# Kernel optimization log

Measured on AMD Instinct MI355X. Metric: run time of the kernel, lower is better.

## Reference

```python
import jax, jax.numpy as jnp
import numpy as np

B, N, DIM = 8, 4096, 1024
H, DH = 16, 64          # heads, dim_head -> inner_dim = 1024
P = 256                 # proj_size (Linformer low-rank seq projection)
SCALE = DH ** -0.5


def setup_inputs() -> dict:
    key = jax.random.key(0)
    ks = jax.random.split(key, 6)
    return {
        "x": jax.random.normal(ks[0], (B, N, DIM), dtype=jnp.float32),
        "Wqkv": jax.random.normal(ks[1], (3 * H * DH, DIM), dtype=jnp.float32) * 0.02,
        "We": jax.random.normal(ks[2], (P, N), dtype=jnp.float32) * 0.02,
        "be": jax.random.normal(ks[3], (P,), dtype=jnp.float32) * 0.02,
        "Wo": jax.random.normal(ks[4], (DIM, H * DH), dtype=jnp.float32) * 0.02,
        "bo": jax.random.normal(ks[5], (DIM,), dtype=jnp.float32) * 0.02,
    }


def reference(x, Wqkv, We, be, Wo, bo):
    b, n, _ = x.shape
    # fused QKV projection (no bias), split, reshape to (b, h, n, d)
    qkv = jnp.einsum('bnc,ec->bne', x, Wqkv)                      # [b, n, 3*h*d]
    q, k, v = jnp.split(qkv, 3, axis=-1)
    tohead = lambda t: t.reshape(b, n, H, DH).transpose(0, 2, 1, 3)
    q, k, v = tohead(q), tohead(k), tohead(v)
    # shared E=F sequence projection: Linear over seq axis n -> p, bias along p
    kp = jnp.einsum('bhnd,pn->bhpd', k, We) + be[None, None, :, None]
    vp = jnp.einsum('bhnd,pn->bhpd', v, We) + be[None, None, :, None]
    dots = jnp.einsum('bhid,bhjd->bhij', q, kp) * SCALE           # [b, h, n, p]
    attn = jax.nn.softmax(dots, axis=-1)
    out = jnp.einsum('bhij,bhjd->bhid', attn, vp)                 # [b, h, n, d]
    out = out.transpose(0, 2, 1, 3).reshape(b, n, H * DH)
    return jnp.einsum('bne,oe->bno', out, Wo) + bo                # [b, n, dim]
```

## Files before the change

kernel.cpp:

```cpp
#include <hip/hip_runtime.h>
#include <hip/hip_bf16.h>


typedef unsigned short bf16u;
typedef __attribute__((ext_vector_type(8))) short short8;
typedef __attribute__((ext_vector_type(4))) float f32x4;

__device__ __forceinline__ unsigned short f2bf(float f) {
    unsigned u = __float_as_uint(f);
    u += 0x7FFF + ((u >> 16) & 1);
    return (unsigned short)(u >> 16);
}

__device__ __forceinline__ f32x4 mfma16(short8 a, short8 b, f32x4 c) {
    return __builtin_amdgcn_mfma_f32_16x16x32_bf16(a, b, c, 0, 0, 0);
}

__global__ void cvt_kernel(const float* __restrict__ in, bf16u* __restrict__ out, int n4) {
    int i = blockIdx.x * blockDim.x + threadIdx.x;
    int stride = gridDim.x * blockDim.x;
    for (int j = i; j < n4; j += stride) {
        float4 v = ((const float4*)in)[j];
        union { bf16u s[4]; uint2 u; } o;
        o.s[0] = f2bf(v.x); o.s[1] = f2bf(v.y); o.s[2] = f2bf(v.z); o.s[3] = f2bf(v.w);
        ((uint2*)out)[j] = o.u;
    }
}

__global__ __launch_bounds__(256) void cvt_transpose_x(const float* __restrict__ x,
                                                       bf16u* __restrict__ Xbf,
                                                       bf16u* __restrict__ XT) {
    __shared__ bf16u T[64][72];
    const int b = blockIdx.z;
    const int n0 = blockIdx.y * 64, c0 = blockIdx.x * 64;
    const int t = threadIdx.x;
    const int cx = t & 15, ry = t >> 4;
#pragma unroll
    for (int p = 0; p < 4; p++) {
        const int nn = p * 16 + ry;
        const size_t g = ((size_t)b * 4096 + n0 + nn) * 1024 + c0 + cx * 4;
        float4 v = *(const float4*)&x[g];
        union { bf16u s[4]; uint2 u; } o;
        o.s[0] = f2bf(v.x); o.s[1] = f2bf(v.y); o.s[2] = f2bf(v.z); o.s[3] = f2bf(v.w);
        *(uint2*)&Xbf[g] = o.u;
#pragma unroll
        for (int j = 0; j < 4; j++) T[cx * 4 + j][nn] = o.s[j];
    }
    __syncthreads();
    const int cc = t >> 2, ch = t & 3;
#pragma unroll
    for (int j = 0; j < 2; j++) {
        const int nch = ch + j * 4;
        short8 vv = *(const short8*)&T[cc][nch * 8];
        *(short8*)&XT[((size_t)b * 1024 + c0 + cc) * 4096 + n0 + nch * 8] = vv;
    }
}

__device__ __forceinline__ void gemm_core_128(const bf16u* __restrict__ Ablk, int ldA,
                                              const bf16u* __restrict__ Bblk, int ldB,
                                              int Kiter, f32x4 (&acc)[4][4]) {
    __shared__ __align__(16) bf16u As[128 * 32];
    __shared__ __align__(16) bf16u Bs[128 * 32];
    const int t = threadIdx.x;
    const int wave = t >> 6, lane = t & 63;
    const int wm = (wave >> 1) * 64, wn = (wave & 1) * 64;
    const int lr = lane & 15, lk = (lane >> 4) * 8;

    for (int kt = 0; kt < Kiter; kt += 32) {
#pragma unroll
        for (int i = 0; i < 2; i++) {
            int c = i * 256 + wave * 64 + lane;
            const bf16u* ga = Ablk + (size_t)(c >> 2) * ldA + kt + (c & 3) * 8;
            const bf16u* gb = Bblk + (size_t)(c >> 2) * ldB + kt + (c & 3) * 8;
            __builtin_amdgcn_global_load_lds(
                (const __attribute__((address_space(1))) unsigned*)ga,
                (__attribute__((address_space(3))) unsigned*)(&As[(i * 256 + wave * 64) * 8]),
                16, 0, 0);
            __builtin_amdgcn_global_load_lds(
                (const __attribute__((address_space(1))) unsigned*)gb,
                (__attribute__((address_space(3))) unsigned*)(&Bs[(i * 256 + wave * 64) * 8]),
                16, 0, 0);
        }
        __syncthreads();
        short8 a[4], b[4];
#pragma unroll
        for (int mi = 0; mi < 4; mi++)
            a[mi] = *(const short8*)&As[(wm + mi * 16 + lr) * 32 + lk];
#pragma unroll
        for (int ni = 0; ni < 4; ni++)
            b[ni] = *(const short8*)&Bs[(wn + ni * 16 + lr) * 32 + lk];
#pragma unroll
        for (int mi = 0; mi < 4; mi++)
#pragma unroll
            for (int ni = 0; ni < 4; ni++)
                acc[mi][ni] = mfma16(a[mi], b[ni], acc[mi][ni]);
        __syncthreads();
    }
}

__global__ __launch_bounds__(256) void gemm_ex_splitk(const bf16u* __restrict__ We,
                                                      const bf16u* __restrict__ XT,
                                                      float* __restrict__ Cpart) {
    const int bn = blockIdx.x, bm = blockIdx.y;
    const int bz = blockIdx.z >> 2, ks = blockIdx.z & 3;
    f32x4 acc[4][4];
#pragma unroll
    for (int i = 0; i < 4; i++)
#pragma unroll
        for (int j = 0; j < 4; j++) acc[i][j] = f32x4{0.f, 0.f, 0.f, 0.f};

    gemm_core_128(We + (size_t)bm * 128 * 4096 + ks * 1024, 4096,
                  XT + ((size_t)bz * 1024 + bn * 128) * 4096 + ks * 1024, 4096,
                  1024, acc);

    const int lane = threadIdx.x & 63, wave = threadIdx.x >> 6;
    const int wm = (wave >> 1) * 64, wn = (wave & 1) * 64;
    const int lr = lane & 15, lg = (lane >> 4) * 4;
    float* Cp = Cpart + (size_t)(ks * 8 + bz) * 256 * 1024;
#pragma unroll
    for (int ni = 0; ni < 4; ni++) {
        const int col = bn * 128 + wn + ni * 16 + lr;
#pragma unroll
        for (int mi = 0; mi < 4; mi++) {
#pragma unroll
            for (int r = 0; r < 4; r++) {
                const int row = bm * 128 + wm + mi * 16 + lg + r;
                Cp[(size_t)row * 1024 + col] = acc[mi][ni][r];
            }
        }
    }
}

__global__ __launch_bounds__(256) void reduce4_cvt(const float* __restrict__ P,
                                                   bf16u* __restrict__ out) {
    const int j = blockIdx.x * blockDim.x + threadIdx.x;
    const float4* p = (const float4*)P;
    float4 s0 = p[j], s1 = p[j + 524288], s2 = p[j + 1048576], s3 = p[j + 1572864];
    union { bf16u s[4]; uint2 u; } o;
    o.s[0] = f2bf((s0.x + s1.x) + (s2.x + s3.x));
    o.s[1] = f2bf((s0.y + s1.y) + (s2.y + s3.y));
    o.s[2] = f2bf((s0.z + s1.z) + (s2.z + s3.z));
    o.s[3] = f2bf((s0.w + s1.w) + (s2.w + s3.w));
    ((uint2*)out)[j] = o.u;
}

__global__ __launch_bounds__(256) void gemm_kpv(const bf16u* __restrict__ EX,
                                                const bf16u* __restrict__ Wkv,
                                                const float* __restrict__ be,
                                                bf16u* __restrict__ kp,
                                                bf16u* __restrict__ vpT) {
    const int bn = blockIdx.x, bm = blockIdx.y, bz = blockIdx.z;
    f32x4 acc[4][4];
#pragma unroll
    for (int i = 0; i < 4; i++)
#pragma unroll
        for (int j = 0; j < 4; j++) acc[i][j] = f32x4{0.f, 0.f, 0.f, 0.f};

    gemm_core_128(EX + (size_t)bz * 256 * 1024 + (size_t)bm * 128 * 1024, 1024,
                  Wkv + (size_t)bn * 128 * 1024, 1024, 1024, acc);

    const int lane = threadIdx.x & 63, wave = threadIdx.x >> 6;
    const int wm = (wave >> 1) * 64, wn = (wave & 1) * 64;
    const int lr = lane & 15, lg = (lane >> 4) * 4;
    bf16u* kpB = kp + (size_t)bz * 256 * 1024;
    bf16u* vpB = vpT + (size_t)bz * 1024 * 256;
    const int ebase = bn * 128 + wn;
#pragma unroll
    for (int ni = 0; ni < 4; ni++) {
        const int col = ebase + ni * 16 + lr;
        const int region = (ebase + ni * 16) >> 10;
#pragma unroll
        for (int mi = 0; mi < 4; mi++) {
            const int p0 = bm * 128 + wm + mi * 16 + lg;
            if (region == 0) {
#pragma unroll
                for (int r = 0; r < 4; r++)
                    kpB[(size_t)(p0 + r) * 1024 + col] = f2bf(acc[mi][ni][r] + be[p0 + r]);
            } else {
                const int d = col - 1024;
                union { bf16u s[4]; uint2 u; } o;
#pragma unroll
                for (int r = 0; r < 4; r++) o.s[r] = f2bf(acc[mi][ni][r] + be[p0 + r]);
                *(uint2*)&vpB[(size_t)d * 256 + p0] = o.u;
            }
        }
    }
}

template<int MODE>
__global__ __launch_bounds__(512, 2) void gemm256(const bf16u* __restrict__ A,
                                                  const bf16u* __restrict__ Bt,
                                                  const float* __restrict__ bias,
                                                  void* __restrict__ Cout,
                                                  int K, int NBN) {
    __shared__ __align__(16) bf16u As[2][256 * 64];
    __shared__ __align__(16) bf16u Bs[2][256 * 64];

    const int nwg = gridDim.x;
    const int bid = blockIdx.x;
    const int logical = (bid & 7) * (nwg >> 3) + (bid >> 3);
    const int bn = logical % NBN, bm = logical / NBN;

    const bf16u* Ablk = A + (size_t)bm * 256 * K;
    const bf16u* Bblk = Bt + (size_t)bn * 256 * K;

    const int t = threadIdx.x;
    const int wid = t >> 6, lane = t & 63;
    const int wm = (wid >> 2) * 128, wn = (wid & 3) * 64;
    const int lr = lane & 15, g4 = lane >> 4;

    f32x4 acc[8][4];
#pragma unroll
    for (int i = 0; i < 8; i++)
#pragma unroll
        for (int j = 0; j < 4; j++) acc[i][j] = f32x4{0.f, 0.f, 0.f, 0.f};

    const int nkt = K >> 6;

#pragma unroll
    for (int i = 0; i < 4; i++) {
        const int c = i * 512 + t;
        const int row = c >> 3, gp = c & 7;
        const int col = (gp ^ (row & 7)) * 8;
        __builtin_amdgcn_global_load_lds(
            (const __attribute__((address_space(1))) unsigned*)(Ablk + (size_t)row * K + col),
            (__attribute__((address_space(3))) unsigned*)(&As[0][c * 8]), 16, 0, 0);
        __builtin_amdgcn_global_load_lds(
            (const __attribute__((address_space(1))) unsigned*)(Bblk + (size_t)row * K + col),
            (__attribute__((address_space(3))) unsigned*)(&Bs[0][c * 8]), 16, 0, 0);
    }
    __syncthreads();

    for (int kt = 0; kt < nkt; kt++) {
        if (kt + 1 < nkt) {
            const int k0 = (kt + 1) * 64;
            bf16u* Ad = As[(kt + 1) & 1];
            bf16u* Bd = Bs[(kt + 1) & 1];
#pragma unroll
            for (int i = 0; i < 4; i++) {
                const int c = i * 512 + t;
                const int row = c >> 3, gp = c & 7;
                const int col = k0 + (gp ^ (row & 7)) * 8;
                __builtin_amdgcn_global_load_lds(
                    (const __attribute__((address_space(1))) unsigned*)(Ablk + (size_t)row * K + col),
                    (__attribute__((address_space(3))) unsigned*)(&Ad[c * 8]), 16, 0, 0);
                __builtin_amdgcn_global_load_lds(
                    (const __attribute__((address_space(1))) unsigned*)(Bblk + (size_t)row * K + col),
                    (__attribute__((address_space(3))) unsigned*)(&Bd[c * 8]), 16, 0, 0);
            }
        }
        const bf16u* Ab = As[kt & 1];
        const bf16u* Bb = Bs[kt & 1];
#pragma unroll
        for (int ks = 0; ks < 2; ks++) {
            short8 a[8], b[4];
#pragma unroll
            for (int mi = 0; mi < 8; mi++) {
                const int row = wm + mi * 16 + lr;
                const int gp = (ks * 4 + g4) ^ (row & 7);
                a[mi] = *(const short8*)&Ab[row * 64 + gp * 8];
            }
#pragma unroll
            for (int ni = 0; ni < 4; ni++) {
                const int row = wn + ni * 16 + lr;
                const int gp = (ks * 4 + g4) ^ (row & 7);
                b[ni] = *(const short8*)&Bb[row * 64 + gp * 8];
            }
#pragma unroll
            for (int mi = 0; mi < 8; mi++)
#pragma unroll
                for (int ni = 0; ni < 4; ni++)
                    acc[mi][ni] = mfma16(a[mi], b[ni], acc[mi][ni]);
        }
        __syncthreads();
    }

    const int lg = g4 * 4;
    const int ldc = NBN * 256;
    if (MODE == 0) {
        bf16u* C = (bf16u*)Cout;
#pragma unroll
        for (int mi = 0; mi < 8; mi++) {
#pragma unroll
            for (int r = 0; r < 4; r++) {
                const size_t row = (size_t)bm * 256 + wm + mi * 16 + lg + r;
#pragma unroll
                for (int ni = 0; ni < 4; ni++)
                    C[row * ldc + bn * 256 + wn + ni * 16 + lr] = f2bf(acc[mi][ni][r]);
            }
        }
    } else {
        float* C = (float*)Cout;
        float bv[4];
#pragma unroll
        for (int ni = 0; ni < 4; ni++) bv[ni] = bias[bn * 256 + wn + ni * 16 + lr];
#pragma unroll
        for (int mi = 0; mi < 8; mi++) {
#pragma unroll
            for (int r = 0; r < 4; r++) {
                const size_t row = (size_t)bm * 256 + wm + mi * 16 + lg + r;
#pragma unroll
                for (int ni = 0; ni < 4; ni++)
                    C[row * ldc + bn * 256 + wn + ni * 16 + lr] = acc[mi][ni][r] + bv[ni];
            }
        }
    }
}

__global__ __launch_bounds__(256, 2) void attn_kernel(const bf16u* __restrict__ Q,
                                                      const bf16u* __restrict__ kp,
                                                      const bf16u* __restrict__ vpT,
                                                      bf16u* __restrict__ O) {
    __shared__ __align__(16) bf16u S[32768];
    const int bh = blockIdx.y, b = bh >> 4, h = bh & 15;
    const int t = threadIdx.x;
    const int wave = t >> 6, lane = t & 63;
    const int lr = lane & 15, g = lane >> 4;
    const int i0 = blockIdx.x * 64 + wave * 16;
    const size_t mrow = (size_t)b * 4096 + i0;

    short8 bq[2];
    const bf16u* Qb = Q + (mrow + lr) * 1024 + h * 64 + g * 8;
    bq[0] = *(const short8*)&Qb[0];
    bq[1] = *(const short8*)&Qb[32];

    const bf16u* kpb = kp + ((size_t)b * 256) * 1024 + h * 64;
    const bf16u* vpb = vpT + ((size_t)b * 1024 + h * 64) * 256;
#pragma unroll
    for (int i = 0; i < 8; i++) {
        const int c = i * 256 + t;
        const int ubase = (i * 256 + wave * 64) * 8;
        {
            const int p = c >> 3, d8 = (c & 7) ^ (p & 7);
            __builtin_amdgcn_global_load_lds(
                (const __attribute__((address_space(1))) unsigned*)(kpb + (size_t)p * 1024 + d8 * 8),
                (__attribute__((address_space(3))) unsigned*)&S[ubase], 16, 0, 0);
        }
        {
            const int d = c >> 5, p8 = (c & 31) ^ (d & 15);
            __builtin_amdgcn_global_load_lds(
                (const __attribute__((address_space(1))) unsigned*)(vpb + (size_t)d * 256 + p8 * 8),
                (__attribute__((address_space(3))) unsigned*)&S[16384 + ubase], 16, 0, 0);
        }
    }
    __syncthreads();

    f32x4 dots[16];
#pragma unroll
    for (int pj = 0; pj < 16; pj++) dots[pj] = f32x4{0.f, 0.f, 0.f, 0.f};
#pragma unroll
    for (int pj = 0; pj < 16; pj++) {
#pragma unroll
        for (int kk = 0; kk < 2; kk++) {
            const int gr = (pj * 16 + lr) * 8 + ((kk * 4 + g) ^ (lr & 7));
            short8 ak = *(const short8*)&S[gr * 8];
            dots[pj] = mfma16(ak, bq[kk], dots[pj]);
        }
    }

    float s = 0.f;
#pragma unroll
    for (int pj = 0; pj < 16; pj++) {
#pragma unroll
        for (int r = 0; r < 4; r++) {
            float e = __expf(dots[pj][r] * 0.125f);
            dots[pj][r] = e;
            s += e;
        }
    }
    s += __shfl_xor(s, 16);
    s += __shfl_xor(s, 32);
    const float inv = 1.0f / s;

    __syncthreads();

    const int pbase = wave * 4096 + lr * 256;
    const int pxor = (lr & 7) << 3;
#pragma unroll
    for (int pj = 0; pj < 16; pj++) {
        unsigned lo = (unsigned)f2bf(dots[pj][0] * inv) | ((unsigned)f2bf(dots[pj][1] * inv) << 16);
        unsigned hi = (unsigned)f2bf(dots[pj][2] * inv) | ((unsigned)f2bf(dots[pj][3] * inv) << 16);
        const int el = (pbase + pj * 16 + g * 4) ^ pxor;
        uint2 u; u.x = lo; u.y = hi;
        *(uint2*)&S[el] = u;
    }

    f32x4 oacc[4];
#pragma unroll
    for (int dj = 0; dj < 4; dj++) oacc[dj] = f32x4{0.f, 0.f, 0.f, 0.f};
#pragma unroll
    for (int pk = 0; pk < 8; pk++) {
        const int el = (pbase + pk * 32 + g * 8) ^ pxor;
        short8 ap = *(const short8*)&S[el];
#pragma unroll
        for (int dj = 0; dj < 4; dj++) {
            const int d = dj * 16 + lr;
            const int gr = d * 32 + ((pk * 4 + g) ^ (d & 15));
            short8 bv = *(const short8*)&S[16384 + gr * 8];
            oacc[dj] = mfma16(ap, bv, oacc[dj]);
        }
    }

    bf16u* Ob = O + (mrow + g * 4) * 1024 + h * 64 + lr;
#pragma unroll
    for (int dj = 0; dj < 4; dj++)
#pragma unroll
        for (int r = 0; r < 4; r++)
            Ob[(size_t)r * 1024 + dj * 16] = f2bf(oacc[dj][r]);
}

extern "C" void kernel_launch(void* const* d_in, const int* in_sizes, int n_in,
                              void* d_out, int out_size, void* d_ws, size_t ws_size,
                              hipStream_t stream) {
    const float* x    = (const float*)d_in[0];
    const float* Wqkv = (const float*)d_in[1];
    const float* We   = (const float*)d_in[2];
    const float* be   = (const float*)d_in[3];
    const float* Wo   = (const float*)d_in[4];
    const float* bo   = (const float*)d_in[5];
    float* out = (float*)d_out;

    char* w = (char*)d_ws;
    bf16u* Qbf  = (bf16u*)(w);
    bf16u* Obuf = (bf16u*)(w + 67108864ull);
    bf16u* Wqb  = (bf16u*)(w + 134217728ull);
    bf16u* Web  = (bf16u*)(w + 140509184ull);
    bf16u* Wob  = (bf16u*)(w + 142606336ull);
    bf16u* EXb  = (bf16u*)(w + 144703488ull);
    if (ws_size < 148897792ull) return;

    bf16u* Xbf = (bf16u*)d_out;
    bf16u* XT  = Xbf + 33554432ull;
    float* EXpart = (float*)d_out;
    bf16u* kpb = Xbf;
    bf16u* vpb = Xbf + 2097152ull;

    cvt_transpose_x<<<dim3(16, 64, 8), 256, 0, stream>>>(x, Xbf, XT);
    cvt_kernel<<<768, 256, 0, stream>>>(Wqkv, Wqb, 3145728 / 4);
    cvt_kernel<<<256, 256, 0, stream>>>(We,   Web, 1048576 / 4);
    cvt_kernel<<<256, 256, 0, stream>>>(Wo,   Wob, 1048576 / 4);

    gemm256<0><<<512, 512, 0, stream>>>(Xbf, Wqb, nullptr, Qbf, 1024, 4);
    gemm_ex_splitk<<<dim3(8, 2, 32), 256, 0, stream>>>(Web, XT, EXpart);
    reduce4_cvt<<<2048, 256, 0, stream>>>(EXpart, EXb);
    gemm_kpv<<<dim3(16, 2, 8), 256, 0, stream>>>(EXb, Wqb + (size_t)1024 * 1024, be, kpb, vpb);

    attn_kernel<<<dim3(64, 128), 256, 0, stream>>>(Qbf, kpb, vpb, Obuf);
    gemm256<1><<<512, 512, 0, stream>>>(Obuf, Wob, bo, out, 1024, 4);
}
```

Baseline: 375.8 us.

## Replace 256x256 GEMM with 256x128 triple-buffered pipelined GEMM with interleaved staging

```diff
diff --git a/kernel.cpp b/kernel.cpp
--- a/kernel.cpp
+++ b/kernel.cpp
@@ -15,6 +15,9 @@
 __device__ __forceinline__ f32x4 mfma16(short8 a, short8 b, f32x4 c) {
     return __builtin_amdgcn_mfma_f32_16x16x32_bf16(a, b, c, 0, 0, 0);
 }
+
+#define AS1 __attribute__((address_space(1)))
+#define AS3 __attribute__((address_space(3)))
 
 __global__ void cvt_kernel(const float* __restrict__ in, bf16u* __restrict__ out, int n4) {
     int i = blockIdx.x * blockDim.x + threadIdx.x;
@@ -72,14 +75,10 @@
             int c = i * 256 + wave * 64 + lane;
             const bf16u* ga = Ablk + (size_t)(c >> 2) * ldA + kt + (c & 3) * 8;
             const bf16u* gb = Bblk + (size_t)(c >> 2) * ldB + kt + (c & 3) * 8;
-            __builtin_amdgcn_global_load_lds(
-                (const __attribute__((address_space(1))) unsigned*)ga,
-                (__attribute__((address_space(3))) unsigned*)(&As[(i * 256 + wave * 64) * 8]),
-                16, 0, 0);
-            __builtin_amdgcn_global_load_lds(
-                (const __attribute__((address_space(1))) unsigned*)gb,
-                (__attribute__((address_space(3))) unsigned*)(&Bs[(i * 256 + wave * 64) * 8]),
-                16, 0, 0);
+            __builtin_amdgcn_global_load_lds((const AS1 unsigned*)ga,
+                (AS3 unsigned*)(&As[(i * 256 + wave * 64) * 8]), 16, 0, 0);
+            __builtin_amdgcn_global_load_lds((const AS1 unsigned*)gb,
+                (AS3 unsigned*)(&Bs[(i * 256 + wave * 64) * 8]), 16, 0, 0);
         }
         __syncthreads();
         short8 a[4], b[4];
@@ -188,120 +187,161 @@
 }
 
 template<int MODE>
-__global__ __launch_bounds__(512, 2) void gemm256(const bf16u* __restrict__ A,
-                                                  const bf16u* __restrict__ Bt,
-                                                  const float* __restrict__ bias,
-                                                  void* __restrict__ Cout,
-                                                  int K, int NBN) {
-    __shared__ __align__(16) bf16u As[2][256 * 64];
-    __shared__ __align__(16) bf16u Bs[2][256 * 64];
+__global__ __launch_bounds__(512, 2) void gemm_deep(const bf16u* __restrict__ A,
+                                                    const bf16u* __restrict__ Bt,
+                                                    const float* __restrict__ bias,
+                                                    void* __restrict__ Cout,
+                                                    int K) {
+    __shared__ __align__(16) bf16u L[3 * 24576];
 
     const int nwg = gridDim.x;
     const int bid = blockIdx.x;
     const int logical = (bid & 7) * (nwg >> 3) + (bid >> 3);
-    const int bn = logical % NBN, bm = logical / NBN;
+    const int bn = logical & 7, bm = logical >> 3;
 
     const bf16u* Ablk = A + (size_t)bm * 256 * K;
-    const bf16u* Bblk = Bt + (size_t)bn * 256 * K;
+    const bf16u* Bblk = Bt + (size_t)bn * 128 * K;
 
     const int t = threadIdx.x;
     const int wid = t >> 6, lane = t & 63;
-    const int wm = (wid >> 2) * 128, wn = (wid & 3) * 64;
+    const int wm = (wid >> 1) * 64, wn = (wid & 1) * 64;
     const int lr = lane & 15, g4 = lane >> 4;
 
-    f32x4 acc[8][4];
-#pragma unroll
-    for (int i = 0; i < 8; i++)
+    f32x4 acc[4][4];
+#pragma unroll
+    for (int i = 0; i < 4; i++)
 #pragma unroll
         for (int j = 0; j < 4; j++) acc[i][j] = f32x4{0.f, 0.f, 0.f, 0.f};
 
+    auto STAGE_A = [&](int buf, int kt, int half) {
+#pragma unroll
+        for (int i = 0; i < 2; i++) {
+            const int c = half * 1024 + i * 512 + t;
+            const int row = c >> 3, gp = c & 7;
+            const int col = kt * 64 + ((gp ^ (row & 7)) << 3);
+            __builtin_amdgcn_global_load_lds(
+                (const AS1 unsigned*)(Ablk + (size_t)row * K + col),
+                (AS3 unsigned*)(&L[buf * 24576 + c * 8]), 16, 0, 0);
+        }
+    };
+    auto STAGE_B = [&](int buf, int kt) {
+#pragma unroll
+        for (int i = 0; i < 2; i++) {
+            const int c = i * 512 + t;
+            const int row = c >> 3, gp = c & 7;
+            const int col = kt * 64 + ((gp ^ (row & 7)) << 3);
+            __builtin_amdgcn_global_load_lds(
+                (const AS1 unsigned*)(Bblk + (size_t)row * K + col),
+                (AS3 unsigned*)(&L[buf * 24576 + 16384 + c * 8]), 16, 0, 0);
+        }
+    };
+
+    short8 aF[2][2], bF[4][2];
+    auto LDA = [&](int buf, int msub) {
+#pragma unroll
+        for (int mi = 0; mi < 2; mi++) {
+            const int R = wm + msub * 32 + mi * 16 + lr;
+#pragma unroll
+            for (int ks = 0; ks < 2; ks++) {
+                const int gp = (ks * 4 + g4) ^ (R & 7);
+                aF[mi][ks] = *(const short8*)&L[buf * 24576 + R * 64 + gp * 8];
+            }
+        }
+    };
+    auto LDB = [&](int buf, int nsub) {
+#pragma unroll
+        for (int ni = 0; ni < 2; ni++) {
+            const int R = wn + nsub * 32 + ni * 16 + lr;
+#pragma unroll
+            for (int ks = 0; ks < 2; ks++) {
+                const int gp = (ks * 4 + g4) ^ (R & 7);
+                bF[nsub * 2 + ni][ks] = *(const short8*)&L[buf * 24576 + 16384 + R * 64 + gp * 8];
+            }
+        }
+    };
+    auto MM = [&](int msub, int nsub) {
+        __builtin_amdgcn_s_setprio(1);
+#pragma unroll
+        for (int mi = 0; mi < 2; mi++)
+#pragma unroll
+            for (int nj = 0; nj < 2; nj++)
+#pragma unroll
+                for (int ks = 0; ks < 2; ks++)
+                    acc[msub * 2 + mi][nsub * 2 + nj] =
+                        mfma16(aF[mi][ks], bF[nsub * 2 + nj][ks], acc[msub * 2 + mi][nsub * 2 + nj]);
+        __builtin_amdgcn_s_setprio(0);
+    };
+    auto BAR = [&]() {
+        asm volatile("" ::: "memory");
+        __builtin_amdgcn_s_barrier();
+        asm volatile("" ::: "memory");
+    };
+    auto WAIT_LGKM0 = [&]() {
+        asm volatile("s_waitcnt lgkmcnt(0)" ::: "memory");
+        __builtin_amdgcn_sched_barrier(0);
+    };
+
     const int nkt = K >> 6;
 
-#pragma unroll
-    for (int i = 0; i < 4; i++) {
-        const int c = i * 512 + t;
-        const int row = c >> 3, gp = c & 7;
-        const int col = (gp ^ (row & 7)) * 8;
-        __builtin_amdgcn_global_load_lds(
-            (const __attribute__((address_space(1))) unsigned*)(Ablk + (size_t)row * K + col),
-            (__attribute__((address_space(3))) unsigned*)(&As[0][c * 8]), 16, 0, 0);
-        __builtin_amdgcn_global_load_lds(
-            (const __attribute__((address_space(1))) unsigned*)(Bblk + (size_t)row * K + col),
-            (__attribute__((address_space(3))) unsigned*)(&Bs[0][c * 8]), 16, 0, 0);
-    }
-    __syncthreads();
-
-    for (int kt = 0; kt < nkt; kt++) {
-        if (kt + 1 < nkt) {
-            const int k0 = (kt + 1) * 64;
-            bf16u* Ad = As[(kt + 1) & 1];
-            bf16u* Bd = Bs[(kt + 1) & 1];
-#pragma unroll
-            for (int i = 0; i < 4; i++) {
-                const int c = i * 512 + t;
-                const int row = c >> 3, gp = c & 7;
-                const int col = k0 + (gp ^ (row & 7)) * 8;
-                __builtin_amdgcn_global_load_lds(
-                    (const __attribute__((address_space(1))) unsigned*)(Ablk + (size_t)row * K + col),
-                    (__attribute__((address_space(3))) unsigned*)(&Ad[c * 8]), 16, 0, 0);
-                __builtin_amdgcn_global_load_lds(
-                    (const __attribute__((address_space(1))) unsigned*)(Bblk + (size_t)row * K + col),
-                    (__attribute__((address_space(3))) unsigned*)(&Bd[c * 8]), 16, 0, 0);
-            }
-        }
-        const bf16u* Ab = As[kt & 1];
-        const bf16u* Bb = Bs[kt & 1];
-#pragma unroll
-        for (int ks = 0; ks < 2; ks++) {
-            short8 a[8], b[4];
-#pragma unroll
-            for (int mi = 0; mi < 8; mi++) {
-                const int row = wm + mi * 16 + lr;
-                const int gp = (ks * 4 + g4) ^ (row & 7);
-                a[mi] = *(const short8*)&Ab[row * 64 + gp * 8];
-            }
-#pragma unroll
-            for (int ni = 0; ni < 4; ni++) {
-                const int row = wn + ni * 16 + lr;
-                const int gp = (ks * 4 + g4) ^ (row & 7);
-                b[ni] = *(const short8*)&Bb[row * 64 + gp * 8];
-            }
-#pragma unroll
-            for (int mi = 0; mi < 8; mi++)
-#pragma unroll
-                for (int ni = 0; ni < 4; ni++)
-                    acc[mi][ni] = mfma16(a[mi], b[ni], acc[mi][ni]);
-        }
-        __syncthreads();
+    STAGE_A(0, 0, 0); STAGE_A(0, 0, 1); STAGE_B(0, 0);
+    STAGE_A(1, 1, 0); STAGE_A(1, 1, 1); STAGE_B(1, 1);
+    asm volatile("s_waitcnt vmcnt(6)" ::: "memory");
+    BAR();
+
+    int cur = 0;
+    for (int j = 0; j < nkt; j++) {
+        const bool stg = (j + 2 < nkt);
+        const int sbuf = (cur >= 1) ? cur - 1 : 2;
+
+        LDA(cur, 0); LDB(cur, 0);
+        if (stg) STAGE_A(sbuf, j + 2, 0);
+        BAR(); WAIT_LGKM0();
+        MM(0, 0);
+        BAR();
+        LDB(cur, 1);
+        if (stg) STAGE_A(sbuf, j + 2, 1);
+        BAR(); WAIT_LGKM0();
+        MM(0, 1);
+        BAR();
+        LDA(cur, 1);
+        if (stg) STAGE_B(sbuf, j + 2);
+        BAR(); WAIT_LGKM0();
+        MM(1, 1);
+        BAR();
+        MM(1, 0);
+        if (j < nkt - 2) asm volatile("s_waitcnt vmcnt(6)" ::: "memory");
+        else             asm volatile("s_waitcnt vmcnt(0)" ::: "memory");
+        BAR();
+
+        cur = (cur == 2) ? 0 : cur + 1;
     }
 
     const int lg = g4 * 4;
-    const int ldc = NBN * 256;
     if (MODE == 0) {
         bf16u* C = (bf16u*)Cout;
 #pragma unroll
-        for (int mi = 0; mi < 8; mi++) {
+        for (int mi = 0; mi < 4; mi++) {
 #pragma unroll
             for (int r = 0; r < 4; r++) {
                 const size_t row = (size_t)bm * 256 + wm + mi * 16 + lg + r;
 #pragma unroll
                 for (int ni = 0; ni < 4; ni++)
-                    C[row * ldc + bn * 256 + wn + ni * 16 + lr] = f2bf(acc[mi][ni][r]);
+                    C[row * 1024 + bn * 128 + wn + ni * 16 + lr] = f2bf(acc[mi][ni][r]);
             }
         }
     } else {
         float* C = (float*)Cout;
         float bv[4];
 #pragma unroll
-        for (int ni = 0; ni < 4; ni++) bv[ni] = bias[bn * 256 + wn + ni * 16 + lr];
-#pragma unroll
-        for (int mi = 0; mi < 8; mi++) {
+        for (int ni = 0; ni < 4; ni++) bv[ni] = bias[bn * 128 + wn + ni * 16 + lr];
+#pragma unroll
+        for (int mi = 0; mi < 4; mi++) {
 #pragma unroll
             for (int r = 0; r < 4; r++) {
                 const size_t row = (size_t)bm * 256 + wm + mi * 16 + lg + r;
 #pragma unroll
                 for (int ni = 0; ni < 4; ni++)
-                    C[row * ldc + bn * 256 + wn + ni * 16 + lr] = acc[mi][ni][r] + bv[ni];
+                    C[row * 1024 + bn * 128 + wn + ni * 16 + lr] = acc[mi][ni][r] + bv[ni];
             }
         }
     }
@@ -333,14 +373,14 @@
         {
             const int p = c >> 3, d8 = (c & 7) ^ (p & 7);
             __builtin_amdgcn_global_load_lds(
-                (const __attribute__((address_space(1))) unsigned*)(kpb + (size_t)p * 1024 + d8 * 8),
-                (__attribute__((address_space(3))) unsigned*)&S[ubase], 16, 0, 0);
+                (const AS1 unsigned*)(kpb + (size_t)p * 1024 + d8 * 8),
+                (AS3 unsigned*)&S[ubase], 16, 0, 0);
         }
         {
             const int d = c >> 5, p8 = (c & 31) ^ (d & 15);
             __builtin_amdgcn_global_load_lds(
-                (const __attribute__((address_space(1))) unsigned*)(vpb + (size_t)d * 256 + p8 * 8),
-                (__attribute__((address_space(3))) unsigned*)&S[16384 + ubase], 16, 0, 0);
+                (const AS1 unsigned*)(vpb + (size_t)d * 256 + p8 * 8),
+                (AS3 unsigned*)&S[16384 + ubase], 16, 0, 0);
         }
     }
     __syncthreads();
@@ -440,11 +480,11 @@
     cvt_kernel<<<256, 256, 0, stream>>>(We,   Web, 1048576 / 4);
     cvt_kernel<<<256, 256, 0, stream>>>(Wo,   Wob, 1048576 / 4);
 
-    gemm256<0><<<512, 512, 0, stream>>>(Xbf, Wqb, nullptr, Qbf, 1024, 4);
+    gemm_deep<0><<<1024, 512, 0, stream>>>(Xbf, Wqb, nullptr, Qbf, 1024);
     gemm_ex_splitk<<<dim3(8, 2, 32), 256, 0, stream>>>(Web, XT, EXpart);
     reduce4_cvt<<<2048, 256, 0, stream>>>(EXpart, EXb);
     gemm_kpv<<<dim3(16, 2, 8), 256, 0, stream>>>(EXb, Wqb + (size_t)1024 * 1024, be, kpb, vpb);
 
     attn_kernel<<<dim3(64, 128), 256, 0, stream>>>(Qbf, kpb, vpb, Obuf);
-    gemm256<1><<<512, 512, 0, stream>>>(Obuf, Wob, bo, out, 1024, 4);
-}
+    gemm_deep<1><<<1024, 512, 0, stream>>>(Obuf, Wob, bo, out, 1024);
+}
```

New measurement: 374.7 us. About the same (-0.3%).
